# Kernel optimization log

Measured on AMD Instinct MI355X. Metric: run time of the kernel, lower is better.

## Reference

```python
import jax, jax.numpy as jnp
import numpy as np

WEIGHT = 1.0  # init kwarg `weight`
BOX = 5      # half-size of the text box in pixels


def setup_inputs() -> dict:
    key = jax.random.key(0)
    k1, k2, k3, k4 = jax.random.split(key, 4)
    B, C, H, W, T = 32, 4, 512, 512, 64
    return {
        "predicted_noise": jax.random.normal(k1, (B, C, H, W), dtype=jnp.float32),
        "target_noise": jax.random.normal(k2, (B, C, H, W), dtype=jnp.float32),
        "text_tokens": jax.random.randint(k3, (B, T), 0, 50000, dtype=jnp.int64),
        "text_positions": jax.random.uniform(k4, (B, T, 2), dtype=jnp.float32),
    }


def _text_mask(text_positions, H, W, dtype):
    # text_positions: [B, T, 2] normalized (x, y). A valid token (x>0, y>0)
    # paints a [y_pos-5, y_pos+5) x [x_pos-5, x_pos+5) box of ones (clipped to image).
    x = text_positions[..., 0]
    y = text_positions[..., 1]
    valid = (x > 0) & (y > 0)                              # [B, T]
    x_pos = jnp.floor(x * W).astype(jnp.int32)             # int(x*W), x>0 so floor==trunc
    y_pos = jnp.floor(y * H).astype(jnp.int32)
    ii = jnp.arange(H, dtype=jnp.int32)                    # rows; clipping is implicit
    jj = jnp.arange(W, dtype=jnp.int32)
    cond_y = valid[..., None] & (ii >= y_pos[..., None] - BOX) & (ii < y_pos[..., None] + BOX)  # [B,T,H]
    cond_x = (jj >= x_pos[..., None] - BOX) & (jj < x_pos[..., None] + BOX)                      # [B,T,W]
    # union over tokens of the outer-product boxes, via a small matmul over T
    hits = jnp.einsum('bti,btj->bij', cond_y.astype(dtype), cond_x.astype(dtype))  # [B,H,W]
    return (hits > 0).astype(dtype)


def reference(predicted_noise, target_noise, text_tokens, text_positions):
    diff2 = (predicted_noise - target_noise) ** 2
    base_loss = jnp.mean(diff2)
    _, _, H, W = predicted_noise.shape
    mask = _text_mask(text_positions, H, W, predicted_noise.dtype)   # [B,H,W]
    text_weight = 1.0 + 3.0 * mask[:, None, :, :]                    # [B,1,H,W]
    text_loss = jnp.mean(text_weight * diff2)
    return base_loss + WEIGHT * (text_loss - base_loss)
```

## Files before the change

### kernel.cpp

```cpp
#include <hip/hip_runtime.h>

#define Bb 32
#define Cc 4
#define Hh 512
#define Ww 512
#define Tt 64
#define HW (Hh * Ww)
#define NTOT ((long long)Bb * Cc * Hh * Ww)
#define QTOT (Bb * Cc * HW / 4)

#define GRID2 2048
#define THREADS2 (GRID2 * 256)
#define ITER_TOT (QTOT / THREADS2)
#define OUTER 4
#define INNER 4

#define ROWMASK_OFF 65536

__global__ __launch_bounds__(256) void build_rowmask_kernel(
    const float* __restrict__ pos,
    unsigned long long* __restrict__ rowmask)
{
    int row = blockIdx.x * 256 + threadIdx.x;
    if (row >= Bb * Hh) return;
    int b = row >> 9;
    int h = row & 511;

    unsigned long long m[8];
#pragma unroll
    for (int i = 0; i < 8; ++i) m[i] = 0ull;

    const float* p = pos + (size_t)b * Tt * 2;
    for (int t = 0; t < Tt; ++t) {
        float x = p[2 * t + 0];
        float y = p[2 * t + 1];
        if (!(x > 0.0f && y > 0.0f)) continue;
        int xp = (int)floorf(x * (float)Ww);
        int yp = (int)floorf(y * (float)Hh);
        if (h < yp - 5 || h >= yp + 5) continue;
        int xlo = xp - 5; if (xlo < 0) xlo = 0;
        int xhi = xp + 5; if (xhi > Ww) xhi = Ww;
        if (xlo >= xhi) continue;
        int w0 = xlo >> 6;
        int w1 = (xhi - 1) >> 6;
        for (int wd = w0; wd <= w1; ++wd) {
            int lo = xlo - (wd << 6); if (lo < 0) lo = 0;
            int hi = xhi - (wd << 6); if (hi > 64) hi = 64;
            m[wd] |= (((1ull << (hi - lo)) - 1ull) << lo);
        }
    }

    unsigned long long* out = rowmask + (size_t)row * 8;
#pragma unroll
    for (int i = 0; i < 8; ++i) out[i] = m[i];
}

__global__ __launch_bounds__(256, 4) void weighted_sq_sum_kernel(
    const float4* __restrict__ pred4,
    const float4* __restrict__ targ4,
    const unsigned long long* __restrict__ rowmask,
    double* __restrict__ partials)
{
    const int tid0 = blockIdx.x * 256 + threadIdx.x;

    double acc = 0.0;
#pragma unroll
    for (int ot = 0; ot < OUTER; ++ot) {
        float4 pa[INNER], ta[INNER];
        unsigned long long wd[INNER];
        unsigned sh[INNER];
#pragma unroll
        for (int it = 0; it < INNER; ++it) {
            int gid = tid0 + (ot * INNER + it) * THREADS2;
            pa[it] = pred4[gid];
            ta[it] = targ4[gid];
            int b     = gid >> 18;
            int h     = (gid >> 7) & 511;
            int wword = (gid >> 4) & 7;
            wd[it] = rowmask[(((size_t)b << 9) + (size_t)h) * 8 + wword];
            sh[it] = (unsigned)((gid & 15) << 2);
        }
#pragma unroll
        for (int it = 0; it < INNER; ++it) {
            float dx = pa[it].x - ta[it].x;
            float dy = pa[it].y - ta[it].y;
            float dz = pa[it].z - ta[it].z;
            float dw = pa[it].w - ta[it].w;
            float sx = dx * dx, sy = dy * dy, sz = dz * dz, sw = dw * dw;
            unsigned bits = (unsigned)((wd[it] >> sh[it]) & 0xFull);
            float tot  = sx + sy + sz + sw;
            float msum = (bits & 1u ? sx : 0.f) + (bits & 2u ? sy : 0.f) +
                         (bits & 4u ? sz : 0.f) + (bits & 8u ? sw : 0.f);
            acc += (double)tot + 3.0 * (double)msum;
        }
    }

#pragma unroll
    for (int off = 32; off > 0; off >>= 1)
        acc += __shfl_down(acc, off, 64);

    __shared__ double lsum[4];
    int lane = threadIdx.x & 63;
    int wid  = threadIdx.x >> 6;
    if (lane == 0) lsum[wid] = acc;
    __syncthreads();
    if (threadIdx.x == 0)
        partials[blockIdx.x] = lsum[0] + lsum[1] + lsum[2] + lsum[3];
}

__global__ __launch_bounds__(256) void final_reduce_kernel(
    const double* __restrict__ partials, float* __restrict__ out)
{
    double v = 0.0;
    for (int i = threadIdx.x; i < GRID2; i += 256) v += partials[i];
#pragma unroll
    for (int off = 32; off > 0; off >>= 1)
        v += __shfl_down(v, off, 64);
    __shared__ double lsum[4];
    int lane = threadIdx.x & 63;
    int wid  = threadIdx.x >> 6;
    if (lane == 0) lsum[wid] = v;
    __syncthreads();
    if (threadIdx.x == 0)
        out[0] = (float)((lsum[0] + lsum[1] + lsum[2] + lsum[3]) * (1.0 / (double)NTOT));
}

extern "C" void kernel_launch(void* const* d_in, const int* in_sizes, int n_in,
                              void* d_out, int out_size, void* d_ws, size_t ws_size,
                              hipStream_t stream) {
    const float* pred = (const float*)d_in[0];
    const float* targ = (const float*)d_in[1];
    const float* pos  = (const float*)d_in[3];

    double* partials = (double*)d_ws;
    unsigned long long* rowmask =
        (unsigned long long*)((char*)d_ws + ROWMASK_OFF);
    float* out = (float*)d_out;

    build_rowmask_kernel<<<(Bb * Hh + 255) / 256, 256, 0, stream>>>(pos, rowmask);

    weighted_sq_sum_kernel<<<GRID2, 256, 0, stream>>>(
        (const float4*)pred, (const float4*)targ, rowmask, partials);

    final_reduce_kernel<<<1, 256, 0, stream>>>(partials, out);
}
```

Measured before the change: 299.7 us.

## Double-buffer loads across outer iterations with a halved grid

Halves the reduction grid and gives each thread twice as many float4 elements. Loads for the next batch of four go into a second register set while the current batch is computed. sched_barrier fences keep the compiler from reordering loads and compute across these stages. The aim is to keep more memory requests in flight per wave and hide HBM latency, at the cost of higher register pressure, which may lower occupancy.

```diff
diff --git a/kernel.cpp b/kernel.cpp
--- a/kernel.cpp
+++ b/kernel.cpp
@@ -9,11 +9,10 @@
 #define NTOT ((long long)Bb * Cc * Hh * Ww)
 #define QTOT (Bb * Cc * HW / 4)
 
-#define GRID2 2048
+#define GRID2 1024
 #define THREADS2 (GRID2 * 256)
-#define ITER_TOT (QTOT / THREADS2)
-#define OUTER 4
-#define INNER 4
+#define NOUTER 8
+#define NBATCH 4
 
 #define ROWMASK_OFF 65536
 
@@ -55,44 +54,61 @@
     for (int i = 0; i < 8; ++i) out[i] = m[i];
 }
 
+#define ROWM(g) rowmask[(((size_t)((g) >> 18) << 9) + (size_t)(((g) >> 7) & 511)) * 8 \
+                        + (size_t)(((g) >> 4) & 7)]
+
 __global__ __launch_bounds__(256, 4) void weighted_sq_sum_kernel(
     const float4* __restrict__ pred4,
     const float4* __restrict__ targ4,
     const unsigned long long* __restrict__ rowmask,
     double* __restrict__ partials)
 {
-    const int tid0 = blockIdx.x * 256 + threadIdx.x;
+    const int tid0 = blockIdx.x * 256 + (int)threadIdx.x;
+
+    float4 pA[NBATCH], tA[NBATCH], pB[NBATCH], tB[NBATCH];
+    unsigned long long wA[NBATCH], wB[NBATCH];
+
+#pragma unroll
+    for (int k = 0; k < NBATCH; ++k) {
+        int g = tid0 + k * THREADS2;
+        pA[k] = pred4[g];
+        tA[k] = targ4[g];
+        wA[k] = ROWM(g);
+    }
+    __builtin_amdgcn_sched_barrier(0);
 
     double acc = 0.0;
 #pragma unroll
-    for (int ot = 0; ot < OUTER; ++ot) {
-        float4 pa[INNER], ta[INNER];
-        unsigned long long wd[INNER];
-        unsigned sh[INNER];
+    for (int ot = 0; ot < NOUTER; ++ot) {
+        const bool evn = ((ot & 1) == 0);
+
+        if (ot + 1 < NOUTER) {
 #pragma unroll
-        for (int it = 0; it < INNER; ++it) {
-            int gid = tid0 + (ot * INNER + it) * THREADS2;
-            pa[it] = pred4[gid];
-            ta[it] = targ4[gid];
-            int b     = gid >> 18;
-            int h     = (gid >> 7) & 511;
-            int wword = (gid >> 4) & 7;
-            wd[it] = rowmask[(((size_t)b << 9) + (size_t)h) * 8 + wword];
-            sh[it] = (unsigned)((gid & 15) << 2);
+            for (int k = 0; k < NBATCH; ++k) {
+                int g = tid0 + ((ot + 1) * NBATCH + k) * THREADS2;
+                if (evn) { pB[k] = pred4[g]; tB[k] = targ4[g]; wB[k] = ROWM(g); }
+                else     { pA[k] = pred4[g]; tA[k] = targ4[g]; wA[k] = ROWM(g); }
+            }
         }
+        __builtin_amdgcn_sched_barrier(0);
+
 #pragma unroll
-        for (int it = 0; it < INNER; ++it) {
-            float dx = pa[it].x - ta[it].x;
-            float dy = pa[it].y - ta[it].y;
-            float dz = pa[it].z - ta[it].z;
-            float dw = pa[it].w - ta[it].w;
+        for (int k = 0; k < NBATCH; ++k) {
+            int g = tid0 + (ot * NBATCH + k) * THREADS2;
+            float4 a             = evn ? pA[k] : pB[k];
+            float4 t             = evn ? tA[k] : tB[k];
+            unsigned long long w = evn ? wA[k] : wB[k];
+            unsigned sh = (unsigned)((g & 15) << 2);
+
+            float dx = a.x - t.x, dy = a.y - t.y, dz = a.z - t.z, dw = a.w - t.w;
             float sx = dx * dx, sy = dy * dy, sz = dz * dz, sw = dw * dw;
-            unsigned bits = (unsigned)((wd[it] >> sh[it]) & 0xFull);
+            unsigned bits = (unsigned)((w >> sh) & 0xFull);
             float tot  = sx + sy + sz + sw;
             float msum = (bits & 1u ? sx : 0.f) + (bits & 2u ? sy : 0.f) +
                          (bits & 4u ? sz : 0.f) + (bits & 8u ? sw : 0.f);
             acc += (double)tot + 3.0 * (double)msum;
         }
+        __builtin_amdgcn_sched_barrier(0);
     }
 
 #pragma unroll
```

New measurement: 289.9 us. -3.3%, faster.
